# Optimization experiments

Measured on AMD Instinct MI355X. Metric: run time of the kernel, lower is better.

The kernel has to match this reference:

```python
import jax, jax.numpy as jnp
import numpy as np
from jax import lax

B, L, EMB, C, H, NTF = 512, 1024, 4, 64, 64, 200
D2 = 2 * H  # 128, bi-LSTM feature dim


def setup_inputs() -> dict:
    key = jax.random.key(0)
    ks = iter(jax.random.split(key, 48))
    r = lambda shape, s=0.05: jax.random.normal(next(ks), shape, jnp.float32) * s
    inp = {"DNA_x": jax.random.normal(next(ks), (B, L, EMB), jnp.float32)}
    # conv stack: channels 4 -> 64 -> 64, kernel 8
    inp["conv0_w"] = r((C, EMB, 8)); inp["conv0_b"] = r((C,))
    inp["bn0_g"] = 1.0 + r((C,)); inp["bn0_b"] = r((C,))
    inp["bn0_m"] = r((C,)); inp["bn0_v"] = jax.random.uniform(next(ks), (C,), jnp.float32, 0.5, 1.5)
    inp["conv1_w"] = r((C, C, 8)); inp["conv1_b"] = r((C,))
    inp["bn1_g"] = 1.0 + r((C,)); inp["bn1_b"] = r((C,))
    inp["bn1_m"] = r((C,)); inp["bn1_v"] = jax.random.uniform(next(ks), (C,), jnp.float32, 0.5, 1.5)
    # bidirectional LSTM, torch gate order (i, f, g, o)
    for d in ("f", "b"):
        inp[f"wih_{d}"] = r((4 * H, C)); inp[f"whh_{d}"] = r((4 * H, H))
        inp[f"bih_{d}"] = r((4 * H,)); inp[f"bhh_{d}"] = r((4 * H,))
    # Bahdanau attention: W1, W2: 128->128, V: 128->NTF
    inp["W1_w"] = r((D2, D2)); inp["W1_b"] = r((D2,))
    inp["W2_w"] = r((D2, D2)); inp["W2_b"] = r((D2,))
    inp["V_w"] = r((NTF, D2)); inp["V_b"] = r((NTF,))
    # per-TF heads stacked: Linear(128->64), Linear(64->1)
    inp["fc1_w"] = r((NTF, 64, D2)); inp["fc1_b"] = r((NTF, 64))
    inp["fc2_w"] = r((NTF, 64)); inp["fc2_b"] = r((NTF,))
    return inp


def _conv(x, w, b):  # x:[B,Cin,L], w:[Cout,Cin,K]
    y = lax.conv_general_dilated(x, w, (1,), "VALID",
                                 dimension_numbers=("NCH", "OIH", "NCH"))
    return y + b[:, None]


def _bn(x, g, b, m, v):  # eval-mode BatchNorm1d over channel dim
    return (x - m[:, None]) * (g[:, None] / jnp.sqrt(v[:, None] + 1e-5)) + b[:, None]


def _lstm(x, Wih, Whh, bih, bhh):  # x:[B,T,D] -> ([B,T,H], h_T:[B,H])
    Bn = x.shape[0]
    Hh = Whh.shape[1]
    bias = bih + bhh
    def step(carry, xt):
        h, c = carry
        g = xt @ Wih.T + h @ Whh.T + bias
        i, f, gg, o = jnp.split(g, 4, axis=-1)
        c = jax.nn.sigmoid(f) * c + jax.nn.sigmoid(i) * jnp.tanh(gg)
        h = jax.nn.sigmoid(o) * jnp.tanh(c)
        return (h, c), h
    init = (jnp.zeros((Bn, Hh), x.dtype), jnp.zeros((Bn, Hh), x.dtype))
    (hT, _), hs = lax.scan(step, init, jnp.swapaxes(x, 0, 1))
    return jnp.swapaxes(hs, 0, 1), hT


def reference(DNA_x, conv0_w, conv0_b, bn0_g, bn0_b, bn0_m, bn0_v,
              conv1_w, conv1_b, bn1_g, bn1_b, bn1_m, bn1_v,
              wih_f, whh_f, bih_f, bhh_f, wih_b, whh_b, bih_b, bhh_b,
              W1_w, W1_b, W2_w, W2_b, V_w, V_b,
              fc1_w, fc1_b, fc2_w, fc2_b):
    x = jnp.swapaxes(DNA_x, 1, 2)                      # [B,EMB,L]
    x = jax.nn.relu(_bn(_conv(x, conv0_w, conv0_b), bn0_g, bn0_b, bn0_m, bn0_v))
    x = lax.reduce_window(x, -jnp.inf, lax.max, (1, 1, 4), (1, 1, 4), "VALID")
    x = jax.nn.relu(_bn(_conv(x, conv1_w, conv1_b), bn1_g, bn1_b, bn1_m, bn1_v))
    x = jnp.swapaxes(x, 1, 2)                          # [B,T,C], T=247
    hf, hTf = _lstm(x, wih_f, whh_f, bih_f, bhh_f)
    hb, hTb = _lstm(x[:, ::-1, :], wih_b, whh_b, bih_b, bhh_b)
    values = jnp.concatenate([hf, hb[:, ::-1, :]], axis=-1)   # [B,T,2H]
    # torch h_n.view(B, 2H) on [2,B,H]: flat reshape (replicated exactly)
    h_n = jnp.stack([hTf, hTb], axis=0).reshape(values.shape[0], -1)
    # Bahdanau attention with NTF query heads
    score = jnp.tanh(values @ W1_w.T + W1_b + (h_n @ W2_w.T + W2_b)[:, None, :]) @ V_w.T + V_b
    aw = jax.nn.softmax(score, axis=1)                 # [B,T,NTF], softmax over time
    context = jnp.einsum("btd,btk->bkd", values, aw)   # [B,NTF,2H]
    # fused per-TF MLP heads: grouped GEMM over NTF
    h1 = jax.nn.relu(jnp.einsum("bkd,kod->bko", context, fc1_w) + fc1_b)
    out = jnp.einsum("bko,ko->bk", h1, fc2_w) + fc2_b  # [B,NTF]
    return out
```

## Files before the change

### kernel.cpp

```cpp
#include <hip/hip_runtime.h>
#include <math.h>

#define BB 512
#define LL 1024
#define EMB 4
#define CC 64
#define NTF 200
#define TT 247
#define LP 254
#define D2 128

typedef __attribute__((ext_vector_type(8))) short short8;
typedef __attribute__((ext_vector_type(4))) float f32x4;
typedef __attribute__((ext_vector_type(4))) unsigned int uint4v;

#define L2E  1.4426950408889634f
#define TL2E 2.8853900817779268f

__device__ __forceinline__ float ex2(float x) {
  return __builtin_amdgcn_exp2f(x);
}
__device__ __forceinline__ float tanh2(float y) {
  return 1.0f - 2.0f * __builtin_amdgcn_rcpf(ex2(y) + 1.0f);
}

__device__ __forceinline__ void lds_barrier() {
  __builtin_amdgcn_s_waitcnt(0xC07F);
  __builtin_amdgcn_s_barrier();
}

__device__ __forceinline__ unsigned short bfr(float f) {
  unsigned u = __builtin_bit_cast(unsigned, f);
  u += 0x7fffu + ((u >> 16) & 1u);
  return (unsigned short)(u >> 16);
}

__global__ __launch_bounds__(256) void k_cvt(const float* __restrict__ w0,
    const float* __restrict__ w1,
    const float* __restrict__ wihf, const float* __restrict__ whhf,
    const float* __restrict__ wihb, const float* __restrict__ whhb,
    const float* __restrict__ bihf, const float* __restrict__ bhhf,
    const float* __restrict__ bihb, const float* __restrict__ bhhb,
    const float* __restrict__ W1w, const float* __restrict__ Vw,
    const float* __restrict__ f1w,
    unsigned short* __restrict__ wbf0, unsigned short* __restrict__ wbf1r,
    unsigned short* __restrict__ wihbf, unsigned short* __restrict__ whhbf,
    float* __restrict__ lbias,
    unsigned short* __restrict__ W1bf, unsigned short* __restrict__ Vbf,
    unsigned short* __restrict__ f1bf)
{
  int i = blockIdx.x * 256 + threadIdx.x;
  if (i < 2048) wbf0[i] = bfr(w0[i]);
  if (i < 32768) {
    int co = i >> 9, k = (i >> 6) & 7, ci = i & 63;
    wbf1r[i] = bfr(w1[co * 512 + ci * 8 + k]);
  }
  if (i < 16384) {
    float s = ((i >> 12) == 2) ? TL2E : L2E;
    wihbf[i] = bfr(wihf[i] * s);
    wihbf[16384 + i] = bfr(wihb[i] * s);
    whhbf[i] = bfr(whhf[i] * s);
    whhbf[16384 + i] = bfr(whhb[i] * s);
    W1bf[i] = bfr(W1w[i]);
  }
  if (i < 26624) {
    int row = i >> 7;
    Vbf[i] = (row < NTF) ? bfr(Vw[i]) : (unsigned short)0;
  }
  if (i < 256) {
    float s = ((i >> 6) == 2) ? TL2E : L2E;
    lbias[i] = (bihf[i] + bhhf[i]) * s;
    lbias[256 + i] = (bihb[i] + bhhb[i]) * s;
  }
  {
    int i4 = i * 4;
    if (i4 < 1638400) {
      float4 v = *(const float4*)(f1w + i4);
      f1bf[i4 + 0] = bfr(v.x);
      f1bf[i4 + 1] = bfr(v.y);
      f1bf[i4 + 2] = bfr(v.z);
      f1bf[i4 + 3] = bfr(v.w);
    }
  }
}

__global__ __launch_bounds__(256) void k_conv0m(const float* __restrict__ x,
    const unsigned short* __restrict__ wbf0,
    const float* __restrict__ b0, const float* __restrict__ g0,
    const float* __restrict__ be0, const float* __restrict__ m0,
    const float* __restrict__ v0, unsigned short* __restrict__ pbf)
{
  int b = blockIdx.x;
  int tid = threadIdx.x;
  __shared__ float xs[71 * 4];
  __shared__ float sc[64], sb[64];
  if (tid < 64) {
    float s = g0[tid] * rsqrtf(v0[tid] + 1e-5f);
    sc[tid] = s;
    sb[tid] = (b0[tid] - m0[tid]) * s + be0[tid];
  }
  int w = tid >> 6, lane = tid & 63, nl = lane & 15, quad = lane >> 4;
  short8 bfb[4];
  #pragma unroll
  for (int nt = 0; nt < 4; ++nt)
    bfb[nt] = __builtin_bit_cast(short8,
        *(const uint4v*)(wbf0 + ((nt * 16 + nl) * 32 + quad * 8)));
  for (int li = 0; li < 4; ++li) {
    int l0 = blockIdx.y * 256 + li * 64;
    for (int j = tid; j < 71; j += 256) {
      int l = l0 + j;
      float4 xv = (l < LL) ? *(const float4*)(x + ((size_t)b * LL + l) * EMB)
                           : make_float4(0.f, 0.f, 0.f, 0.f);
      *(float4*)(xs + j * 4) = xv;
    }
    __syncthreads();
    const float* ap = xs + (w * 16 + nl) * 4 + quad;
    short8 af;
    #pragma unroll
    for (int j = 0; j < 8; ++j) af[j] = (short)bfr(ap[j * 4]);
    f32x4 acc[4];
    #pragma unroll
    for (int nt = 0; nt < 4; ++nt) {
      acc[nt] = (f32x4){0.f, 0.f, 0.f, 0.f};
      acc[nt] = __builtin_amdgcn_mfma_f32_16x16x32_bf16(af, bfb[nt], acc[nt], 0, 0, 0);
    }
    int t = (l0 >> 2) + w * 4 + quad;
    if (t < LP) {
      #pragma unroll
      for (int nt = 0; nt < 4; ++nt) {
        int c = nt * 16 + nl;
        float scc = sc[c], sbc = sb[c];
        float mx = -1e30f;
        #pragma unroll
        for (int r = 0; r < 4; ++r) mx = fmaxf(mx, acc[nt][r] * scc + sbc);
        pbf[((size_t)b * LP + t) * CC + c] = bfr(fmaxf(mx, 0.0f));
      }
    }
    __syncthreads();
  }
}

__global__ __launch_bounds__(256) void k_conv1m(const unsigned short* __restrict__ pbf,
    const unsigned short* __restrict__ wbf1r,
    const float* __restrict__ b1, const float* __restrict__ g1,
    const float* __restrict__ be1, const float* __restrict__ m1,
    const float* __restrict__ v1, unsigned short* __restrict__ x2bf)
{
  int b = blockIdx.x, t0 = blockIdx.y * 64;
  __shared__ __align__(16) unsigned short ps[71 * 72];
  __shared__ float sc[64], sb[64];
  int tid = threadIdx.x;
  for (int j = tid; j < 71 * 32; j += 256) {
    int tl = j >> 5, cu = j & 31;
    int t = t0 + tl;
    unsigned v = (t < LP) ? *(const unsigned*)(pbf + ((size_t)b * LP + t) * CC + cu * 2) : 0u;
    *(unsigned*)(&ps[tl * 72 + cu * 2]) = v;
  }
  if (tid < 64) {
    float s = g1[tid] * rsqrtf(v1[tid] + 1e-5f);
    sc[tid] = s;
    sb[tid] = (b1[tid] - m1[tid]) * s + be1[tid];
  }
  __syncthreads();
  int w = tid >> 6, lane = tid & 63, nl = lane & 15, quad = lane >> 4;
  int tlb = w * 16 + nl;
  f32x4 acc[4];
  #pragma unroll
  for (int nt = 0; nt < 4; ++nt) acc[nt] = (f32x4){0.f, 0.f, 0.f, 0.f};
  #pragma unroll
  for (int k8 = 0; k8 < 8; ++k8) {
    short8 af0 = __builtin_bit_cast(short8,
        *(const uint4v*)(&ps[(tlb + k8) * 72 + 0 + quad * 8]));
    short8 af1 = __builtin_bit_cast(short8,
        *(const uint4v*)(&ps[(tlb + k8) * 72 + 32 + quad * 8]));
    #pragma unroll
    for (int nt = 0; nt < 4; ++nt) {
      int co = nt * 16 + nl;
      short8 bf0 = __builtin_bit_cast(short8,
          *(const uint4v*)(wbf1r + (size_t)co * 512 + k8 * 64 + 0 + quad * 8));
      short8 bf1 = __builtin_bit_cast(short8,
          *(const uint4v*)(wbf1r + (size_t)co * 512 + k8 * 64 + 32 + quad * 8));
      acc[nt] = __builtin_amdgcn_mfma_f32_16x16x32_bf16(af0, bf0, acc[nt], 0, 0, 0);
      acc[nt] = __builtin_amdgcn_mfma_f32_16x16x32_bf16(af1, bf1, acc[nt], 0, 0, 0);
    }
  }
  #pragma unroll
  for (int nt = 0; nt < 4; ++nt) {
    int c = nt * 16 + nl;
    float scc = sc[c], sbc = sb[c];
    #pragma unroll
    for (int r = 0; r < 4; ++r) {
      int t = t0 + w * 16 + quad * 4 + r;
      if (t < TT)
        x2bf[((size_t)b * TT + t) * CC + c] = bfr(fmaxf(acc[nt][r] * scc + sbc, 0.0f));
    }
  }
}

__global__ __launch_bounds__(256) void k_lstm_m(const unsigned short* __restrict__ x2bf,
    const unsigned short* __restrict__ wihbf, const unsigned short* __restrict__ whhbf,
    const float* __restrict__ lbias,
    unsigned short* __restrict__ values, float* __restrict__ hT)
{
  int b0 = blockIdx.x * 16;
  int dir = blockIdx.y;
  int tid = threadIdx.x;
  int w = tid >> 6, lane = tid & 63, l15 = lane & 15, quad = lane >> 4;
  int h0 = w * 16;
  const unsigned short* wih = wihbf + dir * 16384;
  const unsigned short* whh = whhbf + dir * 16384;

  short8 bx[4][2], bh[4][2];
  float bias_v[4];
  #pragma unroll
  for (int g = 0; g < 4; ++g) {
    int row = g * 64 + h0 + l15;
    #pragma unroll
    for (int k = 0; k < 2; ++k) {
      bx[g][k] = __builtin_bit_cast(short8, *(const uint4v*)(wih + row * 64 + k * 32 + quad * 8));
      bh[g][k] = __builtin_bit_cast(short8, *(const uint4v*)(whh + row * 64 + k * 32 + quad * 8));
    }
    bias_v[g] = lbias[dir * 256 + g * 64 + h0 + l15];
  }

  __shared__ __align__(16) unsigned short xls[2][8][16 * 72];
  __shared__ __align__(16) unsigned short hist[8][16 * 72];
  for (int j = tid; j < 16 * 72; j += 256) hist[7][j] = 0;

  int bl = tid >> 4, d4 = tid & 15;
  const unsigned short* xrow = x2bf + ((size_t)(b0 + bl) * TT) * 64 + d4 * 4;

  uint2 xr[8];
  #pragma unroll
  for (int k = 0; k < 8; ++k) {
    int t = dir ? (TT - 1 - k) : k;
    xr[k] = *(const uint2*)(xrow + (size_t)t * 64);
  }
  #pragma unroll
  for (int k = 0; k < 8; ++k)
    *(uint2*)(&xls[0][k][bl * 72 + d4 * 4]) = xr[k];
  #pragma unroll
  for (int k = 0; k < 8; ++k) {
    int s = 8 + k;
    int t = dir ? (TT - 1 - s) : s;
    xr[k] = *(const uint2*)(xrow + (size_t)t * 64);
  }
  __syncthreads();

  float cst[4] = {0.f, 0.f, 0.f, 0.f};
  for (int c = 0; c < 31; ++c) {
    int buf = c & 1;
    #pragma unroll
    for (int sl = 0; sl < 8; ++sl) {
      int hp = (sl + 7) & 7;
      short8 ax0 = __builtin_bit_cast(short8, *(const uint4v*)(&xls[buf][sl][l15 * 72 + quad * 8]));
      short8 ax1 = __builtin_bit_cast(short8, *(const uint4v*)(&xls[buf][sl][l15 * 72 + 32 + quad * 8]));
      short8 ah0 = __builtin_bit_cast(short8, *(const uint4v*)(&hist[hp][l15 * 72 + quad * 8]));
      short8 ah1 = __builtin_bit_cast(short8, *(const uint4v*)(&hist[hp][l15 * 72 + 32 + quad * 8]));
      f32x4 aX[4], aH[4];
      #pragma unroll
      for (int g = 0; g < 4; ++g) {
        aX[g] = (f32x4){bias_v[g], bias_v[g], bias_v[g], bias_v[g]};
        aX[g] = __builtin_amdgcn_mfma_f32_16x16x32_bf16(ax0, bx[g][0], aX[g], 0, 0, 0);
        aX[g] = __builtin_amdgcn_mfma_f32_16x16x32_bf16(ax1, bx[g][1], aX[g], 0, 0, 0);
        aH[g] = (f32x4){0.f, 0.f, 0.f, 0.f};
        aH[g] = __builtin_amdgcn_mfma_f32_16x16x32_bf16(ah0, bh[g][0], aH[g], 0, 0, 0);
        aH[g] = __builtin_amdgcn_mfma_f32_16x16x32_bf16(ah1, bh[g][1], aH[g], 0, 0, 0);
      }
      #pragma unroll
      for (int r = 0; r < 4; ++r) {
        float yi = aX[0][r] + aH[0][r];
        float yf = aX[1][r] + aH[1][r];
        float yg = aX[2][r] + aH[2][r];
        float yo = aX[3][r] + aH[3][r];
        float Fi = ex2(-yi);
        float Ff = ex2(-yf);
        float Eg = ex2(yg);
        float fg = __builtin_amdgcn_rcpf(1.0f + Ff);
        float igg = (Eg - 1.0f) * __builtin_amdgcn_rcpf((1.0f + Fi) * (Eg + 1.0f));
        cst[r] = fg * cst[r] + igg;
        float Fo = ex2(-yo);
        float Ec = ex2(cst[r] * TL2E);
        float hh = (Ec - 1.0f) * __builtin_amdgcn_rcpf((1.0f + Fo) * (Ec + 1.0f));
        hist[sl][(quad * 4 + r) * 72 + h0 + l15] = bfr(hh);
        if (c == 30 && sl == 6) {
          int bglob = b0 + quad * 4 + r;
          hT[((size_t)dir * BB + bglob) * 64 + h0 + l15] = hh;
        }
      }
      lds_barrier();
    }
    uint4v dv[4];
    #pragma unroll
    for (int i = 0; i < 4; ++i) {
      int flat = i * 256 + tid;
      int sl = flat >> 7, wb = (flat >> 3) & 15, c8 = flat & 7;
      dv[i] = *(const uint4v*)(&hist[sl][wb * 72 + c8 * 8]);
    }
    #pragma unroll
    for (int i = 0; i < 4; ++i) {
      int flat = i * 256 + tid;
      int sl = flat >> 7, wb = (flat >> 3) & 15, c8 = flat & 7;
      int s = c * 8 + sl;
      if (s < TT) {
        int t = dir ? (TT - 1 - s) : s;
        *(uint4v*)(values + ((size_t)(b0 + wb) * TT + t) * D2 + dir * 64 + c8 * 8) = dv[i];
      }
    }
    if (c < 30) {
      #pragma unroll
      for (int k = 0; k < 8; ++k)
        *(uint2*)(&xls[1 - buf][k][bl * 72 + d4 * 4]) = xr[k];
      #pragma unroll
      for (int k = 0; k < 8; ++k) {
        int s2 = (c + 2) * 8 + k;
        if (s2 > TT - 1) s2 = TT - 1;
        int t2 = dir ? (TT - 1 - s2) : s2;
        xr[k] = *(const uint2*)(xrow + (size_t)t2 * 64);
      }
    }
    lds_barrier();
  }
}

__global__ __launch_bounds__(128) void k_q2(const float* __restrict__ hT,
    const float* __restrict__ W2, const float* __restrict__ W2b,
    float* __restrict__ q2)
{
  int b = blockIdx.x;
  int tid = threadIdx.x;
  __shared__ float4 hn4[32];
  ((float*)hn4)[tid] = hT[(size_t)b * 128 + tid];
  __syncthreads();
  const float4* w4 = (const float4*)(W2 + (size_t)tid * 128);
  float a = W2b[tid];
  #pragma unroll
  for (int j = 0; j < 32; ++j) {
    float4 w = w4[j]; float4 h = hn4[j];
    a += w.x * h.x + w.y * h.y + w.z * h.z + w.w * h.w;
  }
  q2[(size_t)b * 128 + tid] = a;
}

__global__ __launch_bounds__(256) void k_score_m(const unsigned short* __restrict__ vbf,
    const unsigned short* __restrict__ W1bf, const float* __restrict__ W1b,
    const float* __restrict__ q2, const unsigned short* __restrict__ Vbf,
    const float* __restrict__ Vb, unsigned short* __restrict__ scoreT,
    float* __restrict__ pmax, float* __restrict__ psum)
{
  int b = blockIdx.x, t0 = blockIdx.y * 64;
  int tid = threadIdx.x, w = tid >> 6, lane = tid & 63, l15 = lane & 15, quad = lane >> 4;
  __shared__ unsigned short us[64 * 136];
  __shared__ unsigned short sc2[64 * 213];
  const unsigned short* arow = vbf + ((size_t)b * TT + t0 + w * 16 + l15) * 128;
  short8 ax[4];
  #pragma unroll
  for (int ks = 0; ks < 4; ++ks)
    ax[ks] = __builtin_bit_cast(short8, *(const uint4v*)(arow + ks * 32 + quad * 8));
  #pragma unroll
  for (int nt = 0; nt < 8; ++nt) {
    int n = nt * 16 + l15;
    float base = W1b[n] + q2[(size_t)b * 128 + n];
    f32x4 acc = (f32x4){base, base, base, base};
    #pragma unroll
    for (int ks = 0; ks < 4; ++ks) {
      short8 bf = __builtin_bit_cast(short8,
          *(const uint4v*)(W1bf + (size_t)n * 128 + ks * 32 + quad * 8));
      acc = __builtin_amdgcn_mfma_f32_16x16x32_bf16(ax[ks], bf, acc, 0, 0, 0);
    }
    #pragma unroll
    for (int r = 0; r < 4; ++r)
      us[(w * 16 + quad * 4 + r) * 136 + nt * 16 + l15] = bfr(tanh2(acc[r] * TL2E));
  }
  __syncthreads();
  short8 au[4];
  #pragma unroll
  for (int ks = 0; ks < 4; ++ks)
    au[ks] = __builtin_bit_cast(short8, *(const uint4v*)(&us[(w * 16 + l15) * 136 + ks * 32 + quad * 8]));
  for (int nt2 = 0; nt2 < 13; ++nt2) {
    int n = nt2 * 16 + l15;
    float b2 = (n < NTF) ? Vb[n] : 0.0f;
    f32x4 a2 = (f32x4){b2, b2, b2, b2};
    #pragma unroll
    for (int ks = 0; ks < 4; ++ks) {
      short8 bf = __builtin_bit_cast(short8,
          *(const uint4v*)(Vbf + (size_t)n * 128 + ks * 32 + quad * 8));
      a2 = __builtin_amdgcn_mfma_f32_16x16x32_bf16(au[ks], bf, a2, 0, 0, 0);
    }
    #pragma unroll
    for (int r = 0; r < 4; ++r) {
      int tl = w * 16 + quad * 4 + r;
      sc2[tl * 213 + n] = bfr(a2[r]);
    }
  }
  __syncthreads();
  int tg = tid & 3;
  #pragma unroll
  for (int pp = 0; pp < 4; ++pp) {
    int nrow = pp * 64 + (tid >> 2);
    if (nrow < NTF) {
      unsigned uu[8];
      #pragma unroll
      for (int k2 = 0; k2 < 8; ++k2) {
        unsigned lo = sc2[(tg * 16 + k2 * 2) * 213 + nrow];
        unsigned hi = sc2[(tg * 16 + k2 * 2 + 1) * 213 + nrow];
        uu[k2] = lo | (hi << 16);
      }
      size_t dst = ((size_t)b * 208 + nrow) * 256 + t0 + tg * 16;
      *(uint4v*)(scoreT + dst) = (uint4v){uu[0], uu[1], uu[2], uu[3]};
      *(uint4v*)(scoreT + dst + 8) = (uint4v){uu[4], uu[5], uu[6], uu[7]};
      float pm = -1e30f;
      #pragma unroll
      for (int k2 = 0; k2 < 8; ++k2) {
        unsigned xv = uu[k2];
        int t = t0 + tg * 16 + k2 * 2;
        float a = __builtin_bit_cast(float, xv << 16);
        float c2 = __builtin_bit_cast(float, xv & 0xffff0000u);
        if (t < TT) pm = fmaxf(pm, a);
        if (t + 1 < TT) pm = fmaxf(pm, c2);
      }
      float ps = 0.0f;
      #pragma unroll
      for (int k2 = 0; k2 < 8; ++k2) {
        unsigned xv = uu[k2];
        int t = t0 + tg * 16 + k2 * 2;
        float a = __builtin_bit_cast(float, xv << 16);
        float c2 = __builtin_bit_cast(float, xv & 0xffff0000u);
        if (t < TT) ps += ex2((a - pm) * L2E);
        if (t + 1 < TT) ps += ex2((c2 - pm) * L2E);
      }
      float om = __shfl_xor(pm, 1, 64), os = __shfl_xor(ps, 1, 64);
      float nm = fmaxf(pm, om);
      ps = ps * ex2((pm - nm) * L2E) + os * ex2((om - nm) * L2E);
      pm = nm;
      om = __shfl_xor(pm, 2, 64); os = __shfl_xor(ps, 2, 64);
      nm = fmaxf(pm, om);
      ps = ps * ex2((pm - nm) * L2E) + os * ex2((om - nm) * L2E);
      pm = nm;
      if (tg == 0) {
        pmax[((size_t)b * NTF + nrow) * 4 + blockIdx.y] = pm;
        psum[((size_t)b * NTF + nrow) * 4 + blockIdx.y] = ps;
      }
    }
  }
}

__global__ __launch_bounds__(256) void k_ctx_m(const unsigned short* __restrict__ vbf,
    const unsigned short* __restrict__ scoreT,
    const float* __restrict__ pmax, const float* __restrict__ psum,
    unsigned short* __restrict__ ctxbf)
{
  int b = blockIdx.x;
  int tid = threadIdx.x, w = tid >> 6, lane = tid & 63, l15 = lane & 15, quad = lane >> 4;
  __shared__ __align__(16) unsigned short vt[128 * 264];
  __shared__ float sm[208], sls[208];
  for (int flat = tid; flat < 247 * 64; flat += 256) {
    int t = flat >> 6, dp = flat & 63;
    unsigned v = *(const unsigned*)(vbf + ((size_t)b * TT + t) * D2 + dp * 2);
    vt[(dp * 2) * 264 + t] = (unsigned short)(v & 0xffffu);
    vt[(dp * 2 + 1) * 264 + t] = (unsigned short)(v >> 16);
  }
  for (int j = tid; j < 128 * 9; j += 256) {
    int d = j / 9, t = 247 + (j % 9);
    vt[d * 264 + t] = 0;
  }
  for (int j = tid; j < 208; j += 256) {
    if (j < NTF) {
      const float* pmr = pmax + ((size_t)b * NTF + j) * 4;
      const float* psr = psum + ((size_t)b * NTF + j) * 4;
      float m0 = pmr[0], m1 = pmr[1], m2 = pmr[2], m3 = pmr[3];
      float mm = fmaxf(fmaxf(m0, m1), fmaxf(m2, m3));
      float s = psr[0] * ex2((m0 - mm) * L2E) + psr[1] * ex2((m1 - mm) * L2E)
              + psr[2] * ex2((m2 - mm) * L2E) + psr[3] * ex2((m3 - mm) * L2E);
      sm[j] = mm;
      sls[j] = __builtin_amdgcn_rcpf(s);
    } else {
      sm[j] = 1e30f;
      sls[j] = 0.0f;
    }
  }
  __syncthreads();

  const unsigned short* abase = scoreT + (size_t)b * 208 * 256;
  for (int mi = 0; mi < 4; ++mi) {
    int mt = w + 4 * mi;
    if (mt >= 13) continue;
    const unsigned short* arow = abase + (size_t)(mt * 16 + l15) * 256;
    float mrow = sm[mt * 16 + l15];
    short8 af[8];
    #pragma unroll
    for (int ks = 0; ks < 8; ++ks) {
      uint4v raw = *(const uint4v*)(arow + ks * 32 + quad * 8);
      uint4v pk;
      #pragma unroll
      for (int u = 0; u < 4; ++u) {
        unsigned xv = raw[u];
        int t0 = ks * 32 + quad * 8 + u * 2;
        float a = __builtin_bit_cast(float, xv << 16);
        float cc = __builtin_bit_cast(float, xv & 0xffff0000u);
        float pa = (t0 < TT) ? ex2((a - mrow) * L2E) : 0.0f;
        float pc = (t0 + 1 < TT) ? ex2((cc - mrow) * L2E) : 0.0f;
        pk[u] = (unsigned)bfr(pa) | ((unsigned)bfr(pc) << 16);
      }
      af[ks] = __builtin_bit_cast(short8, pk);
    }
    f32x4 acc[8];
    #pragma unroll
    for (int dt = 0; dt < 8; ++dt) {
      acc[dt] = (f32x4){0.f, 0.f, 0.f, 0.f};
      #pragma unroll
      for (int ks = 0; ks < 8; ++ks) {
        short8 bf = __builtin_bit_cast(short8,
            *(const uint4v*)(&vt[(dt * 16 + l15) * 264 + ks * 32 + quad * 8]));
        acc[dt] = __builtin_amdgcn_mfma_f32_16x16x32_bf16(af[ks], bf, acc[dt], 0, 0, 0);
      }
    }
    #pragma unroll
    for (int r = 0; r < 4; ++r) {
      int n = mt * 16 + quad * 4 + r;
      if (n < NTF) {
        float rs = sls[n];
        #pragma unroll
        for (int dt = 0; dt < 8; ++dt)
          ctxbf[((size_t)n * BB + b) * D2 + dt * 16 + l15] = bfr(acc[dt][r] * rs);
      }
    }
  }
}

__global__ __launch_bounds__(256) void k_heads_m(const unsigned short* __restrict__ ctxbf,
    const unsigned short* __restrict__ f1bf, const float* __restrict__ fc1b,
    const float* __restrict__ fc2w, const float* __restrict__ fc2b,
    float* __restrict__ out)
{
  int n = blockIdx.x;
  int b0 = blockIdx.y * 128;
  int tid = threadIdx.x, w = tid >> 6, lane = tid & 63, l15 = lane & 15, quad = lane >> 4;
  short8 bfr_[4][4];
  float f1bv[4], f2v[4];
  #pragma unroll
  for (int nt = 0; nt < 4; ++nt) {
    int o = nt * 16 + l15;
    #pragma unroll
    for (int ks = 0; ks < 4; ++ks)
      bfr_[nt][ks] = __builtin_bit_cast(short8,
          *(const uint4v*)(f1bf + ((size_t)n * 64 + o) * 128 + ks * 32 + quad * 8));
    f1bv[nt] = fc1b[n * 64 + o];
    f2v[nt] = fc2w[n * 64 + o];
  }
  float f2b = fc2b[n];
  #pragma unroll
  for (int mi = 0; mi < 2; ++mi) {
    int m16 = (w * 2 + mi) * 16;
    const unsigned short* arow = ctxbf + ((size_t)n * BB + (b0 + m16 + l15)) * 128;
    short8 af[4];
    #pragma unroll
    for (int ks = 0; ks < 4; ++ks)
      af[ks] = __builtin_bit_cast(short8, *(const uint4v*)(arow + ks * 32 + quad * 8));
    f32x4 acc[4];
    #pragma unroll
    for (int nt = 0; nt < 4; ++nt) {
      acc[nt] = (f32x4){0.f, 0.f, 0.f, 0.f};
      #pragma unroll
      for (int ks = 0; ks < 4; ++ks)
        acc[nt] = __builtin_amdgcn_mfma_f32_16x16x32_bf16(af[ks], bfr_[nt][ks], acc[nt], 0, 0, 0);
    }
    #pragma unroll
    for (int r = 0; r < 4; ++r) {
      float part = 0.0f;
      #pragma unroll
      for (int nt = 0; nt < 4; ++nt)
        part += fmaxf(acc[nt][r] + f1bv[nt], 0.0f) * f2v[nt];
      part += __shfl_xor(part, 1, 64);
      part += __shfl_xor(part, 2, 64);
      part += __shfl_xor(part, 4, 64);
      part += __shfl_xor(part, 8, 64);
      if (l15 == 0) {
        int bb = b0 + m16 + quad * 4 + r;
        out[(size_t)bb * NTF + n] = part + f2b;
      }
    }
  }
}

extern "C" void kernel_launch(void* const* d_in, const int* in_sizes, int n_in,
                              void* d_out, int out_size, void* d_ws, size_t ws_size,
                              hipStream_t stream)
{
  const float* x    = (const float*)d_in[0];
  const float* c0w  = (const float*)d_in[1];
  const float* c0b  = (const float*)d_in[2];
  const float* g0   = (const float*)d_in[3];
  const float* be0  = (const float*)d_in[4];
  const float* m0   = (const float*)d_in[5];
  const float* v0   = (const float*)d_in[6];
  const float* c1w  = (const float*)d_in[7];
  const float* c1b  = (const float*)d_in[8];
  const float* g1   = (const float*)d_in[9];
  const float* be1  = (const float*)d_in[10];
  const float* m1   = (const float*)d_in[11];
  const float* v1   = (const float*)d_in[12];
  const float* wihf = (const float*)d_in[13];
  const float* whhf = (const float*)d_in[14];
  const float* bihf = (const float*)d_in[15];
  const float* bhhf = (const float*)d_in[16];
  const float* wihb = (const float*)d_in[17];
  const float* whhb = (const float*)d_in[18];
  const float* bihb = (const float*)d_in[19];
  const float* bhhb = (const float*)d_in[20];
  const float* W1w  = (const float*)d_in[21];
  const float* W1b  = (const float*)d_in[22];
  const float* W2w  = (const float*)d_in[23];
  const float* W2b  = (const float*)d_in[24];
  const float* Vw   = (const float*)d_in[25];
  const float* Vb   = (const float*)d_in[26];
  const float* f1w  = (const float*)d_in[27];
  const float* f1b  = (const float*)d_in[28];
  const float* f2w  = (const float*)d_in[29];
  const float* f2b  = (const float*)d_in[30];

  float* ws = (float*)d_ws;
  unsigned short* scoreT = (unsigned short*)ws;
  unsigned short* pbf  = (unsigned short*)ws;
  unsigned short* x2bf = (unsigned short*)(ws + 8323072);
  float* pmax   = ws + 14000000;
  float* psum   = ws + 14500000;
  unsigned short* vbf  = (unsigned short*)(ws + 25292800);
  float* hT     = ws + 33387520;
  float* q2     = ws + 33453056;
  unsigned short* ctxbf = (unsigned short*)(ws + 33620992);
  unsigned short* wbf0  = (unsigned short*)(ws + 46728192);
  unsigned short* wbf1r = (unsigned short*)(ws + 46729216);
  unsigned short* wihbf = (unsigned short*)(ws + 46745600);
  unsigned short* whhbf = (unsigned short*)(ws + 46761984);
  float* lbias          = ws + 46778368;
  unsigned short* W1bf  = (unsigned short*)(ws + 46778880);
  unsigned short* Vbf   = (unsigned short*)(ws + 46787072);
  unsigned short* f1bf  = (unsigned short*)(ws + 46800384);
  float* out    = (float*)d_out;

  k_cvt<<<dim3(1600), 256, 0, stream>>>(c0w, c1w, wihf, whhf, wihb, whhb,
                                        bihf, bhhf, bihb, bhhb, W1w, Vw, f1w,
                                        wbf0, wbf1r, wihbf, whhbf, lbias, W1bf, Vbf, f1bf);
  k_conv0m<<<dim3(BB, 4), 256, 0, stream>>>(x, wbf0, c0b, g0, be0, m0, v0, pbf);
  k_conv1m<<<dim3(BB, 4), 256, 0, stream>>>(pbf, wbf1r, c1b, g1, be1, m1, v1, x2bf);
  k_lstm_m<<<dim3(BB / 16, 2), 256, 0, stream>>>(x2bf, wihbf, whhbf, lbias, vbf, hT);
  k_q2<<<dim3(BB), 128, 0, stream>>>(hT, W2w, W2b, q2);
  k_score_m<<<dim3(BB, 4), 256, 0, stream>>>(vbf, W1bf, W1b, q2, Vbf, Vb, scoreT, pmax, psum);
  k_ctx_m<<<dim3(BB), 256, 0, stream>>>(vbf, scoreT, pmax, psum, ctxbf);
  k_heads_m<<<dim3(NTF, 4), 256, 0, stream>>>(ctxbf, f1bf, f1b, f2w, f2b, out);
}
```

Before: 469.8 us.

## Fuse conv0 into conv1 via shared-memory halo and fold q2 into score kernel

Merges the conv0+BN+ReLU+maxpool kernel into the conv1 kernel. Each block recomputes its 71-row pooled halo straight into shared memory, so the bf16 intermediate no longer makes a round trip through global memory. It also computes the W2 projection of the final hidden state inside the score kernel, removing the separate q2 launch. The cost is recomputing overlapping conv0 halo rows (5 sub-tiles instead of 4 per block), and each of the 4 score blocks per batch now redoes the small 128x128 matvec.

```diff
diff --git a/kernel.cpp b/kernel.cpp
--- a/kernel.cpp
+++ b/kernel.cpp
@@ -84,85 +84,72 @@
   }
 }
 
-__global__ __launch_bounds__(256) void k_conv0m(const float* __restrict__ x,
+__global__ __launch_bounds__(256) void k_convs(const float* __restrict__ x,
     const unsigned short* __restrict__ wbf0,
     const float* __restrict__ b0, const float* __restrict__ g0,
     const float* __restrict__ be0, const float* __restrict__ m0,
-    const float* __restrict__ v0, unsigned short* __restrict__ pbf)
-{
-  int b = blockIdx.x;
-  int tid = threadIdx.x;
-  __shared__ float xs[71 * 4];
-  __shared__ float sc[64], sb[64];
-  if (tid < 64) {
-    float s = g0[tid] * rsqrtf(v0[tid] + 1e-5f);
-    sc[tid] = s;
-    sb[tid] = (b0[tid] - m0[tid]) * s + be0[tid];
-  }
-  int w = tid >> 6, lane = tid & 63, nl = lane & 15, quad = lane >> 4;
-  short8 bfb[4];
-  #pragma unroll
-  for (int nt = 0; nt < 4; ++nt)
-    bfb[nt] = __builtin_bit_cast(short8,
-        *(const uint4v*)(wbf0 + ((nt * 16 + nl) * 32 + quad * 8)));
-  for (int li = 0; li < 4; ++li) {
-    int l0 = blockIdx.y * 256 + li * 64;
-    for (int j = tid; j < 71; j += 256) {
-      int l = l0 + j;
-      float4 xv = (l < LL) ? *(const float4*)(x + ((size_t)b * LL + l) * EMB)
-                           : make_float4(0.f, 0.f, 0.f, 0.f);
-      *(float4*)(xs + j * 4) = xv;
-    }
-    __syncthreads();
-    const float* ap = xs + (w * 16 + nl) * 4 + quad;
-    short8 af;
-    #pragma unroll
-    for (int j = 0; j < 8; ++j) af[j] = (short)bfr(ap[j * 4]);
-    f32x4 acc[4];
-    #pragma unroll
-    for (int nt = 0; nt < 4; ++nt) {
-      acc[nt] = (f32x4){0.f, 0.f, 0.f, 0.f};
-      acc[nt] = __builtin_amdgcn_mfma_f32_16x16x32_bf16(af, bfb[nt], acc[nt], 0, 0, 0);
-    }
-    int t = (l0 >> 2) + w * 4 + quad;
-    if (t < LP) {
-      #pragma unroll
-      for (int nt = 0; nt < 4; ++nt) {
-        int c = nt * 16 + nl;
-        float scc = sc[c], sbc = sb[c];
-        float mx = -1e30f;
-        #pragma unroll
-        for (int r = 0; r < 4; ++r) mx = fmaxf(mx, acc[nt][r] * scc + sbc);
-        pbf[((size_t)b * LP + t) * CC + c] = bfr(fmaxf(mx, 0.0f));
-      }
-    }
-    __syncthreads();
-  }
-}
-
-__global__ __launch_bounds__(256) void k_conv1m(const unsigned short* __restrict__ pbf,
+    const float* __restrict__ v0,
     const unsigned short* __restrict__ wbf1r,
     const float* __restrict__ b1, const float* __restrict__ g1,
     const float* __restrict__ be1, const float* __restrict__ m1,
     const float* __restrict__ v1, unsigned short* __restrict__ x2bf)
 {
   int b = blockIdx.x, t0 = blockIdx.y * 64;
+  int tid = threadIdx.x;
+  __shared__ float xs[71 * 4];
   __shared__ __align__(16) unsigned short ps[71 * 72];
-  __shared__ float sc[64], sb[64];
-  int tid = threadIdx.x;
-  for (int j = tid; j < 71 * 32; j += 256) {
-    int tl = j >> 5, cu = j & 31;
-    int t = t0 + tl;
-    unsigned v = (t < LP) ? *(const unsigned*)(pbf + ((size_t)b * LP + t) * CC + cu * 2) : 0u;
-    *(unsigned*)(&ps[tl * 72 + cu * 2]) = v;
-  }
+  __shared__ float sc0[64], sb0[64], sc1[64], sb1[64];
   if (tid < 64) {
-    float s = g1[tid] * rsqrtf(v1[tid] + 1e-5f);
-    sc[tid] = s;
-    sb[tid] = (b1[tid] - m1[tid]) * s + be1[tid];
-  }
-  __syncthreads();
+    float s = g0[tid] * rsqrtf(v0[tid] + 1e-5f);
+    sc0[tid] = s;
+    sb0[tid] = (b0[tid] - m0[tid]) * s + be0[tid];
+    float s1 = g1[tid] * rsqrtf(v1[tid] + 1e-5f);
+    sc1[tid] = s1;
+    sb1[tid] = (b1[tid] - m1[tid]) * s1 + be1[tid];
+  }
   int w = tid >> 6, lane = tid & 63, nl = lane & 15, quad = lane >> 4;
+  short8 bfb[4];
+  #pragma unroll
+  for (int nt = 0; nt < 4; ++nt)
+    bfb[nt] = __builtin_bit_cast(short8,
+        *(const uint4v*)(wbf0 + ((nt * 16 + nl) * 32 + quad * 8)));
+
+  for (int li = 0; li < 5; ++li) {
+    int l0 = t0 * 4 + li * 64;
+    for (int j = tid; j < 71; j += 256) {
+      int l = l0 + j;
+      float4 xv = (l < LL) ? *(const float4*)(x + ((size_t)b * LL + l) * EMB)
+                           : make_float4(0.f, 0.f, 0.f, 0.f);
+      *(float4*)(xs + j * 4) = xv;
+    }
+    __syncthreads();
+    const float* ap = xs + (w * 16 + nl) * 4 + quad;
+    short8 af;
+    #pragma unroll
+    for (int j = 0; j < 8; ++j) af[j] = (short)bfr(ap[j * 4]);
+    f32x4 acc[4];
+    #pragma unroll
+    for (int nt = 0; nt < 4; ++nt) {
+      acc[nt] = (f32x4){0.f, 0.f, 0.f, 0.f};
+      acc[nt] = __builtin_amdgcn_mfma_f32_16x16x32_bf16(af, bfb[nt], acc[nt], 0, 0, 0);
+    }
+    int tl = li * 16 + w * 4 + quad;
+    if (tl < 71) {
+      int t = t0 + tl;
+      #pragma unroll
+      for (int nt = 0; nt < 4; ++nt) {
+        int c = nt * 16 + nl;
+        float scc = sc0[c], sbc = sb0[c];
+        float mx = -1e30f;
+        #pragma unroll
+        for (int r = 0; r < 4; ++r) mx = fmaxf(mx, acc[nt][r] * scc + sbc);
+        float pv = (t < LP) ? fmaxf(mx, 0.0f) : 0.0f;
+        ps[tl * 72 + c] = bfr(pv);
+      }
+    }
+    __syncthreads();
+  }
+
   int tlb = w * 16 + nl;
   f32x4 acc[4];
   #pragma unroll
@@ -187,7 +174,7 @@
   #pragma unroll
   for (int nt = 0; nt < 4; ++nt) {
     int c = nt * 16 + nl;
-    float scc = sc[c], sbc = sb[c];
+    float scc = sc1[c], sbc = sb1[c];
     #pragma unroll
     for (int r = 0; r < 4; ++r) {
       int t = t0 + w * 16 + quad * 4 + r;
@@ -323,28 +310,11 @@
   }
 }
 
-__global__ __launch_bounds__(128) void k_q2(const float* __restrict__ hT,
-    const float* __restrict__ W2, const float* __restrict__ W2b,
-    float* __restrict__ q2)
-{
-  int b = blockIdx.x;
-  int tid = threadIdx.x;
-  __shared__ float4 hn4[32];
-  ((float*)hn4)[tid] = hT[(size_t)b * 128 + tid];
-  __syncthreads();
-  const float4* w4 = (const float4*)(W2 + (size_t)tid * 128);
-  float a = W2b[tid];
-  #pragma unroll
-  for (int j = 0; j < 32; ++j) {
-    float4 w = w4[j]; float4 h = hn4[j];
-    a += w.x * h.x + w.y * h.y + w.z * h.z + w.w * h.w;
-  }
-  q2[(size_t)b * 128 + tid] = a;
-}
-
 __global__ __launch_bounds__(256) void k_score_m(const unsigned short* __restrict__ vbf,
     const unsigned short* __restrict__ W1bf, const float* __restrict__ W1b,
-    const float* __restrict__ q2, const unsigned short* __restrict__ Vbf,
+    const float* __restrict__ hT, const float* __restrict__ W2,
+    const float* __restrict__ W2b,
+    const unsigned short* __restrict__ Vbf,
     const float* __restrict__ Vb, unsigned short* __restrict__ scoreT,
     float* __restrict__ pmax, float* __restrict__ psum)
 {
@@ -352,15 +322,30 @@
   int tid = threadIdx.x, w = tid >> 6, lane = tid & 63, l15 = lane & 15, quad = lane >> 4;
   __shared__ unsigned short us[64 * 136];
   __shared__ unsigned short sc2[64 * 213];
+  __shared__ float hn[128], q2s[128];
+  if (tid < 128) hn[tid] = hT[(size_t)b * 128 + tid];
+  __syncthreads();
+  if (tid < 128) {
+    const float4* w4 = (const float4*)(W2 + (size_t)tid * 128);
+    const float4* h4 = (const float4*)hn;
+    float a = W2b[tid];
+    #pragma unroll
+    for (int j = 0; j < 32; ++j) {
+      float4 wv = w4[j]; float4 hv = h4[j];
+      a += wv.x * hv.x + wv.y * hv.y + wv.z * hv.z + wv.w * hv.w;
+    }
+    q2s[tid] = a;
+  }
   const unsigned short* arow = vbf + ((size_t)b * TT + t0 + w * 16 + l15) * 128;
   short8 ax[4];
   #pragma unroll
   for (int ks = 0; ks < 4; ++ks)
     ax[ks] = __builtin_bit_cast(short8, *(const uint4v*)(arow + ks * 32 + quad * 8));
+  __syncthreads();
   #pragma unroll
   for (int nt = 0; nt < 8; ++nt) {
     int n = nt * 16 + l15;
-    float base = W1b[n] + q2[(size_t)b * 128 + n];
+    float base = W1b[n] + q2s[n];
     f32x4 acc = (f32x4){base, base, base, base};
     #pragma unroll
     for (int ks = 0; ks < 4; ++ks) {
@@ -621,13 +606,11 @@
 
   float* ws = (float*)d_ws;
   unsigned short* scoreT = (unsigned short*)ws;
-  unsigned short* pbf  = (unsigned short*)ws;
   unsigned short* x2bf = (unsigned short*)(ws + 8323072);
   float* pmax   = ws + 14000000;
   float* psum   = ws + 14500000;
   unsigned short* vbf  = (unsigned short*)(ws + 25292800);
   float* hT     = ws + 33387520;
-  float* q2     = ws + 33453056;
   unsigned short* ctxbf = (unsigned short*)(ws + 33620992);
   unsigned short* wbf0  = (unsigned short*)(ws + 46728192);
   unsigned short* wbf1r = (unsigned short*)(ws + 46729216);
@@ -642,11 +625,11 @@
   k_cvt<<<dim3(1600), 256, 0, stream>>>(c0w, c1w, wihf, whhf, wihb, whhb,
                                         bihf, bhhf, bihb, bhhb, W1w, Vw, f1w,
                                         wbf0, wbf1r, wihbf, whhbf, lbias, W1bf, Vbf, f1bf);
-  k_conv0m<<<dim3(BB, 4), 256, 0, stream>>>(x, wbf0, c0b, g0, be0, m0, v0, pbf);
-  k_conv1m<<<dim3(BB, 4), 256, 0, stream>>>(pbf, wbf1r, c1b, g1, be1, m1, v1, x2bf);
+  k_convs<<<dim3(BB, 4), 256, 0, stream>>>(x, wbf0, c0b, g0, be0, m0, v0,
+                                           wbf1r, c1b, g1, be1, m1, v1, x2bf);
   k_lstm_m<<<dim3(BB / 16, 2), 256, 0, stream>>>(x2bf, wihbf, whhbf, lbias, vbf, hT);
-  k_q2<<<dim3(BB), 128, 0, stream>>>(hT, W2w, W2b, q2);
-  k_score_m<<<dim3(BB, 4), 256, 0, stream>>>(vbf, W1bf, W1b, q2, Vbf, Vb, scoreT, pmax, psum);
+  k_score_m<<<dim3(BB, 4), 256, 0, stream>>>(vbf, W1bf, W1b, hT, W2w, W2b,
+                                             Vbf, Vb, scoreT, pmax, psum);
   k_ctx_m<<<dim3(BB), 256, 0, stream>>>(vbf, scoreT, pmax, psum, ctxbf);
   k_heads_m<<<dim3(NTF, 4), 256, 0, stream>>>(ctxbf, f1bf, f1b, f2w, f2b, out);
 }
```

New measurement: 469.2 us. No clear change (-0.1%).
